# Performance work log

Measured on AMD Instinct MI355X. Metric: run time of the kernel, lower is better.

The kernel has to match this reference:

```python
import jax, jax.numpy as jnp
import numpy as np

D_MODEL = 1024
NUM_HEADS = 16
HEAD_DIM = D_MODEL // NUM_HEADS


def setup_inputs() -> dict:
    key = jax.random.key(0)
    k_x, k_wqkv, k_bqkv, k_wo, k_bo = jax.random.split(key, 5)
    x = jax.random.normal(k_x, (2, 2048, D_MODEL), dtype=jnp.float32)
    s = 1.0 / np.sqrt(D_MODEL)
    W_qkv = jax.random.uniform(k_wqkv, (D_MODEL, 3 * D_MODEL), jnp.float32, -s, s)
    b_qkv = jax.random.uniform(k_bqkv, (3 * D_MODEL,), jnp.float32, -s, s)
    W_o = jax.random.uniform(k_wo, (D_MODEL, D_MODEL), jnp.float32, -s, s)
    b_o = jax.random.uniform(k_bo, (D_MODEL,), jnp.float32, -s, s)
    return {"x": x, "W_qkv": W_qkv, "b_qkv": b_qkv, "W_o": W_o, "b_o": b_o}


def reference(x, W_qkv, b_qkv, W_o, b_o):
    B, S, D = x.shape
    # fused QKV projection: [B,S,3D]
    qkv = jnp.einsum('bsd,de->bse', x, W_qkv) + b_qkv
    # [B,S,H,3*hd] -> [B,H,S,3*hd]
    qkv = qkv.reshape(B, S, NUM_HEADS, 3 * HEAD_DIM).transpose(0, 2, 1, 3)
    q, k, v = jnp.split(qkv, 3, axis=-1)  # each [B,H,S,hd]
    scale = 1.0 / jnp.sqrt(jnp.asarray(HEAD_DIM, dtype=x.dtype))
    scores = jnp.einsum('bhqd,bhkd->bhqk', q, k) * scale  # [B,H,S,S]
    attn = jax.nn.softmax(scores, axis=-1)
    values = jnp.einsum('bhqk,bhkd->bhqd', attn, v)  # [B,H,S,hd]
    values = values.transpose(0, 2, 1, 3).reshape(B, S, D)
    out = jnp.einsum('bsd,de->bse', values, W_o) + b_o
    return out
```

## Files before the change

kernel.cpp:

```cpp
#include <hip/hip_runtime.h>
#include <stdint.h>
#include <stddef.h>

typedef _Float16 f16;
typedef _Float16 f16x8 __attribute__((ext_vector_type(8)));
typedef _Float16 f16x4 __attribute__((ext_vector_type(4)));
typedef float    f32x2 __attribute__((ext_vector_type(2)));
typedef float    f32x4 __attribute__((ext_vector_type(4)));
typedef float    f32x16 __attribute__((ext_vector_type(16)));
typedef int      i32x4 __attribute__((ext_vector_type(4)));
typedef int      i32x2 __attribute__((ext_vector_type(2)));

#define S_LEN 2048
#define DM    1024
#define NH    16
#define HD    64
#define NTOK  4096
#define NQKV  3072
#define QSCALE 0.18033688011112042f

#if __has_builtin(__builtin_amdgcn_exp2f)
#define EXP2(x) __builtin_amdgcn_exp2f(x)
#else
#define EXP2(x) __expf((x) * 0.69314718055994531f)
#endif

__device__ __forceinline__ void gl_lds16(const void* g, void* l) {
  __builtin_amdgcn_global_load_lds(
      (const __attribute__((address_space(1))) void*)g,
      (__attribute__((address_space(3))) void*)l, 16, 0, 0);
}

__device__ __forceinline__ void pl32_swap(int& a, int& b) {
#if __has_builtin(__builtin_amdgcn_permlane32_swap)
  i32x2 r = __builtin_amdgcn_permlane32_swap(a, b, false, false);
  a = r.x; b = r.y;
#else
  asm volatile("v_permlane32_swap_b32 %0, %1" : "+v"(a), "+v"(b));
#endif
}

__device__ __forceinline__ float swap_half(float x, int hi) {
  int a = __builtin_bit_cast(int, x);
  int b = a;
  pl32_swap(a, b);
  return __builtin_bit_cast(float, hi ? a : b);
}

__device__ __forceinline__ int pkrtz(float a, float b) {
  auto h = __builtin_amdgcn_cvt_pkrtz(a, b);
  return __builtin_bit_cast(int, h);
}

__device__ __forceinline__ f16x8 mk_frag(int a, int b, int c, int d) {
  i32x4 v = {a, b, c, d};
  return __builtin_bit_cast(f16x8, v);
}

__device__ __forceinline__ f32x2 pk2(const f32x16& v, int i) {
  f32x2 r = {v[2*i], v[2*i+1]};
  return r;
}

__global__ __launch_bounds__(256) void cvt_f16_kernel(const float* __restrict__ in,
                                                      f16* __restrict__ out, int n) {
  int i = (blockIdx.x * 256 + threadIdx.x) * 8;
  if (i >= n) return;
  float4 a = *(const float4*)(in + i);
  float4 b = *(const float4*)(in + i + 4);
  f16x8 v = {(f16)a.x,(f16)a.y,(f16)a.z,(f16)a.w,(f16)b.x,(f16)b.y,(f16)b.z,(f16)b.w};
  *(f16x8*)(out + i) = v;
}

__global__ __launch_bounds__(256) void cvt_tr_kernel(const float* __restrict__ in,
                                                     f16* __restrict__ out, int R, int C) {
  __shared__ float t[32][33];
  int c0 = blockIdx.x * 32, r0 = blockIdx.y * 32;
  int tx = threadIdx.x, ty = threadIdx.y;
  #pragma unroll
  for (int i = 0; i < 4; ++i)
    t[ty + i*8][tx] = in[(size_t)(r0 + ty + i*8) * C + c0 + tx];
  __syncthreads();
  #pragma unroll
  for (int i = 0; i < 4; ++i)
    out[(size_t)(c0 + ty + i*8) * R + r0 + tx] = (f16)t[tx][ty + i*8];
}

template<int EPI>
__global__ __launch_bounds__(256) void gemm128_kernel(
    const f16* __restrict__ A, const f16* __restrict__ Bt,
    const float* __restrict__ bias,
    f16* __restrict__ qb, f16* __restrict__ kb, f16* __restrict__ vtb,
    float* __restrict__ out)
{
  __shared__ f16 As[128*32];
  __shared__ f16 Bs[128*32];
  const int tid = threadIdx.x;
  const int wid = tid >> 6, lane = tid & 63;
  const int g = lane >> 4, r = lane & 15;
  const int flat = blockIdx.x;
  const int xcd = flat & 7, idx = flat >> 3;
  const int m0 = (xcd * 4 + (idx & 3)) * 128;
  const int n0 = (idx >> 2) * 128;
  const int wm = (wid >> 1) * 64, wn = (wid & 1) * 64;

  f32x4 acc[4][4] = {};
  const int srow = tid >> 2;
  const int sch  = tid & 3;

  for (int kt = 0; kt < DM/32; ++kt) {
    const int k0 = kt * 32;
    __syncthreads();
    #pragma unroll
    for (int c = 0; c < 2; ++c) {
      int row = c*64 + srow;
      int sw = (sch ^ ((row >> 1) & 3)) * 8;
      gl_lds16(A  + (size_t)(m0 + row) * DM + k0 + sw, (char*)As + c*4096 + tid*16);
      gl_lds16(Bt + (size_t)(n0 + row) * DM + k0 + sw, (char*)Bs + c*4096 + tid*16);
    }
    __syncthreads();
    f16x8 a[4], b[4];
    #pragma unroll
    for (int mt = 0; mt < 4; ++mt) {
      int rl = wm + mt*16 + r;
      a[mt] = *(const f16x8*)(As + rl*32 + ((g ^ ((rl >> 1) & 3)) * 8));
    }
    #pragma unroll
    for (int nt = 0; nt < 4; ++nt) {
      int cl = wn + nt*16 + r;
      b[nt] = *(const f16x8*)(Bs + cl*32 + ((g ^ ((cl >> 1) & 3)) * 8));
    }
    #pragma unroll
    for (int mt = 0; mt < 4; ++mt)
      #pragma unroll
      for (int nt = 0; nt < 4; ++nt)
        acc[mt][nt] = __builtin_amdgcn_mfma_f32_16x16x32_f16(a[mt], b[nt], acc[mt][nt], 0, 0, 0);
  }

  if (EPI == 0) {
    #pragma unroll
    for (int mt = 0; mt < 4; ++mt) {
      int row0 = m0 + wm + mt*16 + g*4;
      int b_ = row0 >> 11, s0 = row0 & 2047;
      #pragma unroll
      for (int nt = 0; nt < 4; ++nt) {
        int col = n0 + wn + nt*16 + r;
        float bv = bias[col];
        int h = col / 192;
        int cc = col - h*192;
        int which = cc >> 6, d = cc & 63;
        size_t bh = (size_t)(b_*NH + h);
        if (which == 2) {
          f16x4 v;
          #pragma unroll
          for (int i = 0; i < 4; ++i) v[i] = (f16)(acc[mt][nt][i] + bv);
          *(f16x4*)(vtb + (bh*HD + d)*S_LEN + s0) = v;
        } else if (which == 0) {
          #pragma unroll
          for (int i = 0; i < 4; ++i)
            qb[(bh*S_LEN + s0 + i)*HD + d] = (f16)((acc[mt][nt][i] + bv) * QSCALE);
        } else {
          #pragma unroll
          for (int i = 0; i < 4; ++i)
            kb[(bh*S_LEN + s0 + i)*HD + d] = (f16)(acc[mt][nt][i] + bv);
        }
      }
    }
  } else {
    #pragma unroll
    for (int mt = 0; mt < 4; ++mt) {
      int row0 = m0 + wm + mt*16 + g*4;
      #pragma unroll
      for (int nt = 0; nt < 4; ++nt) {
        int col = n0 + wn + nt*16 + r;
        float bv = bias[col];
        #pragma unroll
        for (int i = 0; i < 4; ++i)
          out[(size_t)(row0 + i)*DM + col] = acc[mt][nt][i] + bv;
      }
    }
  }
}

__global__ __launch_bounds__(256) void attn_kernel(
    const f16* __restrict__ qb, const f16* __restrict__ kb,
    const f16* __restrict__ vtb, f16* __restrict__ values)
{
  __shared__ __align__(16) char smem[49664];

  const int tid = threadIdx.x;
  const int wid = tid >> 6, lane = tid & 63;
  const int ql = lane & 31, hi = lane >> 5;
  const int flat = blockIdx.x;
  const int xcd = flat & 7, idx = flat >> 3;
  const int bh = xcd * 4 + (idx & 3);
  const int q0 = (idx >> 2) * 128 + wid * 32;
  const f16* qh = qb  + (size_t)bh * S_LEN * HD;
  const f16* kh = kb  + (size_t)bh * S_LEN * HD;
  const f16* vh = vtb + (size_t)bh * HD * S_LEN;

  int koff[2], voff[2];
  #pragma unroll
  for (int c = 0; c < 2; ++c) {
    int ca = tid + c*256, pr = ca >> 4, pc = ca & 15, lc = pc ^ (pr & 15);
    int row2 = pr*2 + (lc >> 3), e8 = (lc & 7) * 8;
    koff[c] = row2 * HD + e8;
    voff[c] = row2 * S_LEN + e8;
  }

  f16x8 qf[4];
  #pragma unroll
  for (int dk = 0; dk < 4; ++dk)
    qf[dk] = *(const f16x8*)(qh + (size_t)(q0 + ql)*HD + dk*16 + hi*8);

  const int r0b = (ql >> 1) << 8;
  const int xv  = (ql >> 1) & 15;
  const int hb  = ((ql & 1) << 3) | hi;

  f32x2 lacc = {0.f, 0.f};
  f32x16 o0 = {}, o1 = {};
  f32x16 sX0, sX1, sY0, sY1;

  #define STAGE_K(kt_, buf_) do {                                          \
    const f16* ks_ = kh + (size_t)((kt_)*64) * HD;                         \
    char* kd_ = smem + (buf_)*8192;                                        \
    gl_lds16(ks_ + koff[0], kd_ + tid*16);                                 \
    gl_lds16(ks_ + koff[1], kd_ + 4096 + tid*16);                          \
  } while (0)
  #define STAGE_V(kt_, buf_) do {                                          \
    const f16* vs_ = vh + (kt_)*64;                                        \
    char* vd_ = smem + 16384*2 + (buf_)*8192;                              \
    gl_lds16(vs_ + voff[0], vd_ + tid*16);                                 \
    gl_lds16(vs_ + voff[1], vd_ + 4096 + tid*16);                          \
  } while (0)

  #define QK_H(S_, KsC_, base_) do {                                       \
    S_ = (f32x16){};                                                       \
    _Pragma("unroll")                                                      \
    for (int dk = 0; dk < 4; ++dk) {                                       \
      int off = r0b + (((hb | (dk << 1)) ^ xv) << 4);                      \
      f16x8 kf = *(const f16x8*)((KsC_) + (base_) + off);                  \
      S_ = __builtin_amdgcn_mfma_f32_32x32x16_f16(kf, qf[dk], S_, 0, 0, 0);\
    }                                                                      \
  } while (0)

  #define EXP_H(S_, PFA_, PFB_) do {                                       \
    _Pragma("unroll")                                                      \
    for (int i = 0; i < 16; ++i) S_[i] = EXP2(S_[i]);                      \
    f32x2 sm[4];                                                           \
    _Pragma("unroll")                                                      \
    for (int i = 0; i < 4; ++i) sm[i] = pk2(S_, i) + pk2(S_, i + 4);       \
    sm[0] += sm[1]; sm[2] += sm[3]; lacc += sm[0] + sm[2];                 \
    int a = pkrtz(S_[0], S_[1]), b = pkrtz(S_[2], S_[3]);                  \
    int c = pkrtz(S_[4], S_[5]), d = pkrtz(S_[6], S_[7]);                  \
    pl32_swap(a, c); pl32_swap(b, d);                                      \
    PFA_ = mk_frag(a, b, c, d);                                            \
    a = pkrtz(S_[8],  S_[9]);  b = pkrtz(S_[10], S_[11]);                  \
    c = pkrtz(S_[12], S_[13]); d = pkrtz(S_[14], S_[15]);                  \
    pl32_swap(a, c); pl32_swap(b, d);                                      \
    PFB_ = mk_frag(a, b, c, d);                                            \
  } while (0)

  #define PVQ(buf_) do {                                                   \
    const char* VsC = smem + 16384*2 + (buf_)*8192;                        \
    __builtin_amdgcn_s_setprio(1);                                         \
    _Pragma("unroll")                                                      \
    for (int w = 0; w < 4; ++w) {                                          \
      int off = r0b + (((hb | (w << 1)) ^ xv) << 4);                       \
      f16x8 vf0 = *(const f16x8*)(VsC + off);                              \
      f16x8 vf1 = *(const f16x8*)(VsC + 4096 + off);                       \
      o0 = __builtin_amdgcn_mfma_f32_32x32x16_f16(pf[w], vf0, o0, 0, 0, 0);\
      o1 = __builtin_amdgcn_mfma_f32_32x32x16_f16(pf[w], vf1, o1, 0, 0, 0);\
    }                                                                      \
    __builtin_amdgcn_s_setprio(0);                                         \
  } while (0)

  #define BODY(SA0_, SA1_, SB0_, SB1_, kt_) do {                           \
    const char* KsN = smem + (((kt_) + 1) & 3)*8192;                       \
    const int kst_ = ((kt_) + 4 > 31) ? 31 : ((kt_) + 4);                  \
    STAGE_V((kt_) + 1, ((kt_) + 1) & 1);                                   \
    STAGE_K(kst_, (kt_) & 3);                                              \
    QK_H(SB0_, KsN, 0);                                                    \
    EXP_H(SA0_, pf[0], pf[1]);                                             \
    QK_H(SB1_, KsN, 4096);                                                 \
    EXP_H(SA1_, pf[2], pf[3]);                                             \
    PVQ((kt_) & 1);                                                        \
    asm volatile("s_waitcnt vmcnt(2)" ::: "memory");                       \
    __builtin_amdgcn_s_barrier();                                          \
    __builtin_amdgcn_sched_barrier(0);                                     \
  } while (0)

  STAGE_K(0, 0); STAGE_V(0, 0); STAGE_K(1, 1); STAGE_K(2, 2); STAGE_K(3, 3);
  __syncthreads();
  f16x8 pf[4];
  QK_H(sX0, smem, 0);
  QK_H(sX1, smem, 4096);
  __syncthreads();

  for (int kt2 = 0; kt2 < 30; kt2 += 2) {
    BODY(sX0, sX1, sY0, sY1, kt2);
    BODY(sY0, sY1, sX0, sX1, kt2 + 1);
  }
  BODY(sX0, sX1, sY0, sY1, 30);
  EXP_H(sY0, pf[0], pf[1]);
  EXP_H(sY1, pf[2], pf[3]);
  PVQ(1);

  #undef STAGE_K
  #undef STAGE_V
  #undef QK_H
  #undef EXP_H
  #undef PVQ
  #undef BODY

  float l_run = lacc.x + lacc.y;
  l_run += swap_half(l_run, hi);
  float inv = 1.0f / l_run;
  float* cb = (float*)(smem + 49152) + wid*32;
  __syncthreads();
  cb[ql] = inv;
  __syncthreads();
  f32x4 vinv[4];
  #pragma unroll
  for (int t = 0; t < 4; ++t)
    vinv[t] = *(const f32x4*)(cb + hi*4 + t*8);

  const int b_ = bh >> 4, h = bh & 15;
  #pragma unroll
  for (int t = 0; t < 4; ++t)
    #pragma unroll
    for (int i = 0; i < 4; ++i) {
      int qrow = q0 + 4*hi + 8*t + i;
      size_t base = (size_t)(b_*S_LEN + qrow) * DM + h*HD + ql;
      values[base]      = (f16)(o0[t*4+i] * vinv[t][i]);
      values[base + 32] = (f16)(o1[t*4+i] * vinv[t][i]);
    }
}

extern "C" void kernel_launch(void* const* d_in, const int* in_sizes, int n_in,
                              void* d_out, int out_size, void* d_ws, size_t ws_size,
                              hipStream_t stream) {
  (void)in_sizes; (void)n_in; (void)out_size; (void)ws_size;
  const float* x    = (const float*)d_in[0];
  const float* Wqkv = (const float*)d_in[1];
  const float* bqkv = (const float*)d_in[2];
  const float* Wo   = (const float*)d_in[3];
  const float* bo   = (const float*)d_in[4];
  float* out = (float*)d_out;

  char* ws = (char*)d_ws;
  f16* x_h    = (f16*)(ws);
  f16* Wqkv_t = (f16*)(ws + ( 8ull<<20));
  f16* Wo_t   = (f16*)(ws + (14ull<<20));
  f16* qbuf   = (f16*)(ws + (16ull<<20));
  f16* kbuf   = (f16*)(ws + (24ull<<20));
  f16* vtbuf  = (f16*)(ws + (32ull<<20));
  f16* vals   = (f16*)(ws + (40ull<<20));

  cvt_f16_kernel<<<dim3(NTOK*DM/8/256), dim3(256), 0, stream>>>(x, x_h, NTOK*DM);
  cvt_tr_kernel<<<dim3(NQKV/32, DM/32), dim3(32, 8), 0, stream>>>(Wqkv, Wqkv_t, DM, NQKV);
  cvt_tr_kernel<<<dim3(DM/32, DM/32),  dim3(32, 8), 0, stream>>>(Wo, Wo_t, DM, DM);

  gemm128_kernel<0><<<dim3(768), dim3(256), 0, stream>>>(
      x_h, Wqkv_t, bqkv, qbuf, kbuf, vtbuf, nullptr);

  attn_kernel<<<dim3(512), dim3(256), 0, stream>>>(qbuf, kbuf, vtbuf, vals);

  gemm128_kernel<1><<<dim3(256), dim3(256), 0, stream>>>(
      vals, Wo_t, bo, nullptr, nullptr, nullptr, out);
}
```

Before: 118.2 us.

## Double-buffer GEMM LDS tiles and seed QK MFMA with a zero accumulator

The 128x128 GEMM now keeps two LDS buffers for the A and B tiles. It issues the global-to-LDS load for the next k-tile before computing on the current one, replacing the two barriers per iteration with one. This is meant to overlap global memory latency with the MFMA work, at the cost of twice the LDS per block, which may lower occupancy. In attention, the first QK MFMA now takes a constant zero accumulator, so the explicit zeroing of the score registers is dropped.

```diff
diff --git a/kernel.cpp b/kernel.cpp
--- a/kernel.cpp
+++ b/kernel.cpp
@@ -93,8 +93,8 @@
     f16* __restrict__ qb, f16* __restrict__ kb, f16* __restrict__ vtb,
     float* __restrict__ out)
 {
-  __shared__ f16 As[128*32];
-  __shared__ f16 Bs[128*32];
+  __shared__ f16 As[2][128*32];
+  __shared__ f16 Bs[2][128*32];
   const int tid = threadIdx.x;
   const int wid = tid >> 6, lane = tid & 63;
   const int g = lane >> 4, r = lane & 15;
@@ -107,35 +107,48 @@
   f32x4 acc[4][4] = {};
   const int srow = tid >> 2;
   const int sch  = tid & 3;
+  int soff[2];
+  #pragma unroll
+  for (int c = 0; c < 2; ++c) {
+    int row = c*64 + srow;
+    soff[c] = (size_t)0 + row * DM + ((sch ^ ((row >> 1) & 3)) * 8);
+  }
+  const f16* Ab = A  + (size_t)m0 * DM;
+  const f16* Bb = Bt + (size_t)n0 * DM;
+
+  #define G_STAGE(kt_, buf_) do {                                              \
+    _Pragma("unroll")                                                          \
+    for (int c = 0; c < 2; ++c) {                                              \
+      gl_lds16(Ab + (kt_)*32 + soff[c], (char*)As[buf_] + c*4096 + tid*16);    \
+      gl_lds16(Bb + (kt_)*32 + soff[c], (char*)Bs[buf_] + c*4096 + tid*16);    \
+    }                                                                          \
+  } while (0)
+
+  G_STAGE(0, 0);
+  __syncthreads();
 
   for (int kt = 0; kt < DM/32; ++kt) {
-    const int k0 = kt * 32;
-    __syncthreads();
-    #pragma unroll
-    for (int c = 0; c < 2; ++c) {
-      int row = c*64 + srow;
-      int sw = (sch ^ ((row >> 1) & 3)) * 8;
-      gl_lds16(A  + (size_t)(m0 + row) * DM + k0 + sw, (char*)As + c*4096 + tid*16);
-      gl_lds16(Bt + (size_t)(n0 + row) * DM + k0 + sw, (char*)Bs + c*4096 + tid*16);
-    }
-    __syncthreads();
+    const int cur = kt & 1;
+    if (kt + 1 < DM/32) G_STAGE(kt + 1, cur ^ 1);
     f16x8 a[4], b[4];
     #pragma unroll
     for (int mt = 0; mt < 4; ++mt) {
       int rl = wm + mt*16 + r;
-      a[mt] = *(const f16x8*)(As + rl*32 + ((g ^ ((rl >> 1) & 3)) * 8));
+      a[mt] = *(const f16x8*)(As[cur] + rl*32 + ((g ^ ((rl >> 1) & 3)) * 8));
     }
     #pragma unroll
     for (int nt = 0; nt < 4; ++nt) {
       int cl = wn + nt*16 + r;
-      b[nt] = *(const f16x8*)(Bs + cl*32 + ((g ^ ((cl >> 1) & 3)) * 8));
+      b[nt] = *(const f16x8*)(Bs[cur] + cl*32 + ((g ^ ((cl >> 1) & 3)) * 8));
     }
     #pragma unroll
     for (int mt = 0; mt < 4; ++mt)
       #pragma unroll
       for (int nt = 0; nt < 4; ++nt)
         acc[mt][nt] = __builtin_amdgcn_mfma_f32_16x16x32_f16(a[mt], b[nt], acc[mt][nt], 0, 0, 0);
-  }
+    __syncthreads();
+  }
+  #undef G_STAGE
 
   if (EPI == 0) {
     #pragma unroll
@@ -220,6 +233,7 @@
   f32x2 lacc = {0.f, 0.f};
   f32x16 o0 = {}, o1 = {};
   f32x16 sX0, sX1, sY0, sY1;
+  const f32x16 ZERO = {};
 
   #define STAGE_K(kt_, buf_) do {                                          \
     const f16* ks_ = kh + (size_t)((kt_)*64) * HD;                         \
@@ -235,9 +249,13 @@
   } while (0)
 
   #define QK_H(S_, KsC_, base_) do {                                       \
-    S_ = (f32x16){};                                                       \
+    {                                                                      \
+      int off0 = r0b + ((hb ^ xv) << 4);                                   \
+      f16x8 kf0 = *(const f16x8*)((KsC_) + (base_) + off0);                \
+      S_ = __builtin_amdgcn_mfma_f32_32x32x16_f16(kf0, qf[0], ZERO, 0, 0, 0);\
+    }                                                                      \
     _Pragma("unroll")                                                      \
-    for (int dk = 0; dk < 4; ++dk) {                                       \
+    for (int dk = 1; dk < 4; ++dk) {                                       \
       int off = r0b + (((hb | (dk << 1)) ^ xv) << 4);                      \
       f16x8 kf = *(const f16x8*)((KsC_) + (base_) + off);                  \
       S_ = __builtin_amdgcn_mfma_f32_32x32x16_f16(kf, qf[dk], S_, 0, 0, 0);\
```

After: 128.5 us. 1.09x slower.
